# Performance work log

Measured on AMD Instinct MI355X. Metric: run time of the kernel, lower is better.

The kernel has to match this reference:

```python
import jax, jax.numpy as jnp
import numpy as np

N, E, F, C, K, H = 100000, 1600000, 64, 32, 8, 36


def setup_inputs() -> dict:
    key = jax.random.key(0)
    ks = jax.random.split(key, 24)
    s = 0.1
    inp = {
        "x": jax.random.normal(ks[0], (N, F), jnp.float32),
        "edge_index": jax.random.randint(ks[1], (2, E), 0, N, dtype=jnp.int32),
        # ChebConv conv1_1: K x [F, H] weights + bias
        "W1_1": jax.random.normal(ks[2], (K, F, H), jnp.float32) * s,
        "b1_1": jnp.zeros((H,), jnp.float32),
        "g1_1": jnp.ones((H,), jnp.float32),
        "be1_1": jnp.zeros((H,), jnp.float32),
        # ChebConv conv1_2: K x [H, H]
        "W1_2": jax.random.normal(ks[3], (K, H, H), jnp.float32) * s,
        "b1_2": jnp.zeros((H,), jnp.float32),
        "g1_2": jnp.ones((H,), jnp.float32),
        "be1_2": jnp.zeros((H,), jnp.float32),
        # GINConv MLP: Linear(F,H) -> ReLU -> Linear(H,H)
        "gin_w1": jax.random.normal(ks[4], (F, H), jnp.float32) * s,
        "gin_b1": jnp.zeros((H,), jnp.float32),
        "gin_w2": jax.random.normal(ks[5], (H, H), jnp.float32) * s,
        "gin_b2": jnp.zeros((H,), jnp.float32),
        "g2": jnp.ones((H,), jnp.float32),
        "be2": jnp.zeros((H,), jnp.float32),
        # conv4: ChebConv K=1 on concat(3H) -> C  (pure linear, no propagation)
        "W4": jax.random.normal(ks[6], (1, 3 * H, C), jnp.float32) * s,
        "b4": jnp.zeros((C,), jnp.float32),
    }
    return inp


def _spmm(w, src, dst, x, n):
    # out[i] = sum_{e: dst_e=i} w_e * x[src_e]
    return jax.ops.segment_sum(w[:, None] * x[src], dst, num_segments=n)


def _cheb(x, src, dst, w, Wk, b):
    # PyG ChebConv with sym norm, lambda_max=2: L_hat = -D^-1/2 A D^-1/2 (loop weight 0)
    n = x.shape[0]
    Kk = Wk.shape[0]
    Tx0 = x
    out = Tx0 @ Wk[0]
    if Kk > 1:
        Tx1 = _spmm(w, src, dst, Tx0, n)
        out = out + Tx1 @ Wk[1]
        for k in range(2, Kk):
            Tx2 = 2.0 * _spmm(w, src, dst, Tx1, n) - Tx0
            out = out + Tx2 @ Wk[k]
            Tx0, Tx1 = Tx1, Tx2
    return out + b


def _bn(x, g, b, eps=1e-5):
    m = jnp.mean(x, axis=0)
    v = jnp.mean(jnp.square(x - m), axis=0)  # biased var, training-mode BN
    return g * (x - m) * jax.lax.rsqrt(v + eps) + b


def reference(x, edge_index, W1_1, b1_1, g1_1, be1_1, W1_2, b1_2, g1_2, be1_2,
              gin_w1, gin_b1, gin_w2, gin_b2, g2, be2, W4, b4):
    src, dst = edge_index[0], edge_index[1]
    n = x.shape[0]
    deg = jax.ops.segment_sum(jnp.ones((src.shape[0],), x.dtype), src, num_segments=n)
    dis = jnp.where(deg > 0, jax.lax.rsqrt(jnp.maximum(deg, 1.0)), 0.0)
    w = -dis[src] * dis[dst]  # scaled Laplacian edge weights

    x1_1 = jax.nn.relu(_bn(_cheb(x, src, dst, w, W1_1, b1_1), g1_1, be1_1))
    x1_2 = jax.nn.relu(_bn(_cheb(x1_1, src, dst, w, W1_2, b1_2), g1_2, be1_2))

    # GINConv (eps=0): nn(x + sum_{j in N(i)} x_j)
    agg = jax.ops.segment_sum(x[src], dst, num_segments=n)
    h = x + agg
    gin = jax.nn.relu(h @ gin_w1 + gin_b1) @ gin_w2 + gin_b2
    x2 = _bn(jax.nn.relu(gin), g2, be2)

    x4 = jnp.concatenate((x1_1, x1_2, x2), axis=1)
    return x4 @ W4[0] + b4
```

## Files before the change

### kernel.cpp

```cpp
#include <hip/hip_runtime.h>

constexpr int N_NODES = 100000;
constexpr int N_EDGES = 1600000;
constexpr int NBK  = 391;
constexpr int NBLK = 640;
constexpr int CHUNK = 2500;
constexpr int LCNT = NBK * NBLK;
constexpr int SCAN_BLKS = (LCNT + 255) / 256;


__device__ __forceinline__ unsigned bf16pack(float a, float b) {
    unsigned ua = __float_as_uint(a), ub = __float_as_uint(b);
    ua += 0x7fffu + ((ua >> 16) & 1u);
    ub += 0x7fffu + ((ub >> 16) & 1u);
    return (ua >> 16) | (ub & 0xffff0000u);
}
__device__ __forceinline__ float bflo(unsigned p) { return __uint_as_float(p << 16); }
__device__ __forceinline__ float bfhi(unsigned p) { return __uint_as_float(p & 0xffff0000u); }

__device__ __forceinline__ int esrc(unsigned v) { return (int)(v & 0x1FFFFu); }
__device__ __forceinline__ float ew(unsigned v) {
    return __uint_as_float(0x80000000u | ((v >> 17) << 16));
}

__device__ __forceinline__ size_t sidx(int c, int row) {
    return (c < 8) ? ((size_t)row * 8 + c) : ((size_t)N_NODES * 8 + row);
}


__global__ __launch_bounds__(256) void part_count_kernel(
    const int* __restrict__ ei, int* __restrict__ cntD, int* __restrict__ cntS) {
    __shared__ int hd[NBK], hs[NBK];
    int tid = threadIdx.x;
    for (int i = tid; i < NBK; i += 256) { hd[i] = 0; hs[i] = 0; }
    __syncthreads();
    int e0 = blockIdx.x * CHUNK;
    for (int e = e0 + tid; e < e0 + CHUNK; e += 256) {
        int s = ei[e], d = ei[N_EDGES + e];
        atomicAdd(&hs[s >> 8], 1);
        atomicAdd(&hd[d >> 8], 1);
    }
    __syncthreads();
    for (int i = tid; i < NBK; i += 256) {
        cntD[i * NBLK + blockIdx.x] = hd[i];
        cntS[i * NBLK + blockIdx.x] = hs[i];
    }
}

__global__ __launch_bounds__(256) void scanA_kernel(const int* __restrict__ in,
                                                    int* __restrict__ out,
                                                    int* __restrict__ bsum, int L) {
    __shared__ int sm[256];
    int i = blockIdx.x * 256 + threadIdx.x;
    int v = (i < L) ? in[i] : 0;
    sm[threadIdx.x] = v;
    __syncthreads();
    for (int off = 1; off < 256; off <<= 1) {
        int t = (threadIdx.x >= off) ? sm[threadIdx.x - off] : 0;
        __syncthreads();
        sm[threadIdx.x] += t;
        __syncthreads();
    }
    if (i < L) out[i] = sm[threadIdx.x] - v;
    if (threadIdx.x == 255) bsum[blockIdx.x] = sm[255];
}

__global__ __launch_bounds__(1024) void scanB_kernel(int* __restrict__ bsum, int nb) {
    __shared__ int sm[1024];
    int t = threadIdx.x;
    int v = (t < nb) ? bsum[t] : 0;
    sm[t] = v;
    __syncthreads();
    for (int off = 1; off < 1024; off <<= 1) {
        int u = (t >= off) ? sm[t - off] : 0;
        __syncthreads();
        sm[t] += u;
        __syncthreads();
    }
    if (t < nb) bsum[t] = sm[t] - v;
}

__global__ __launch_bounds__(256) void scanC_kernel(int* __restrict__ out,
                                                    const int* __restrict__ bsum, int L) {
    int i = blockIdx.x * 256 + threadIdx.x;
    if (i < L) out[i] += bsum[blockIdx.x];
}

__global__ __launch_bounds__(256) void part_scatter_kernel(
    const int* __restrict__ ei, const int* __restrict__ scanD,
    const int* __restrict__ scanS, int2* __restrict__ edgepart,
    int* __restrict__ srcpart) {
    __shared__ int curD[NBK], curS[NBK];
    int tid = threadIdx.x;
    for (int i = tid; i < NBK; i += 256) {
        curD[i] = scanD[i * NBLK + blockIdx.x];
        curS[i] = scanS[i * NBLK + blockIdx.x];
    }
    __syncthreads();
    int e0 = blockIdx.x * CHUNK;
    for (int e = e0 + tid; e < e0 + CHUNK; e += 256) {
        int s = ei[e], d = ei[N_EDGES + e];
        int pd = atomicAdd(&curD[d >> 8], 1);
        edgepart[pd] = make_int2(s, d);
        int ps = atomicAdd(&curS[s >> 8], 1);
        srcpart[ps] = s;
    }
}

__global__ __launch_bounds__(256) void deg_kernel(const int* __restrict__ srcpart,
                                                  const int* __restrict__ scanS,
                                                  float* __restrict__ dis) {
    __shared__ int cnt[256];
    int b = blockIdx.x, tid = threadIdx.x;
    cnt[tid] = 0;
    __syncthreads();
    int beg = scanS[b * NBLK];
    int end = (b + 1 < NBK) ? scanS[(b + 1) * NBLK] : N_EDGES;
    for (int j = beg + tid; j < end; j += 256)
        atomicAdd(&cnt[srcpart[j] & 255], 1);
    __syncthreads();
    int node = b * 256 + tid;
    if (node < N_NODES) dis[node] = cnt[tid] > 0 ? rsqrtf((float)cnt[tid]) : 0.f;
}

__global__ __launch_bounds__(256) void csr_kernel(const int2* __restrict__ edgepart,
                                                  const int* __restrict__ scanD,
                                                  const float* __restrict__ dis,
                                                  int* __restrict__ rp,
                                                  unsigned* __restrict__ csrc) {
    __shared__ int cnt[256];
    __shared__ int lofs[256];
    __shared__ float disl[256];
    int b = blockIdx.x, tid = threadIdx.x;
    int beg = scanD[b * NBLK];
    int end = (b + 1 < NBK) ? scanD[(b + 1) * NBLK] : N_EDGES;
    int node = b * 256 + tid;
    cnt[tid] = 0;
    disl[tid] = (node < N_NODES) ? dis[node] : 0.f;
    __syncthreads();
    for (int j = beg + tid; j < end; j += 256)
        atomicAdd(&cnt[edgepart[j].y & 255], 1);
    __syncthreads();
    int v = cnt[tid];
    lofs[tid] = v;
    __syncthreads();
    for (int off = 1; off < 256; off <<= 1) {
        int t = (tid >= off) ? lofs[tid - off] : 0;
        __syncthreads();
        lofs[tid] += t;
        __syncthreads();
    }
    int myexc = lofs[tid] - v;
    if (node < N_NODES) rp[node] = beg + myexc;
    if (b == NBK - 1 && tid == 0) rp[N_NODES] = N_EDGES;
    __syncthreads();
    lofs[tid] = myexc;
    cnt[tid] = 0;
    __syncthreads();
    for (int j = beg + tid; j < end; j += 256) {
        int2 e = edgepart[j];
        int dl = e.y & 255;
        int pos = beg + lofs[dl] + atomicAdd(&cnt[dl], 1);
        unsigned u = __float_as_uint(-(dis[e.x] * disl[dl]));
        u += 0x7fffu + ((u >> 16) & 1u);
        unsigned wb = (u >> 16) & 0x7FFFu;
        csrc[pos] = (unsigned)e.x | (wb << 17);
    }
}

__global__ void pack_x_kernel(const float* __restrict__ x, uint2* __restrict__ xbf) {
    int i = blockIdx.x * blockDim.x + threadIdx.x;
    if (i >= N_NODES * 16) return;
    float4 v = ((const float4*)x)[i];
    xbf[i] = make_uint2(bf16pack(v.x, v.y), bf16pack(v.z, v.w));
}


template <int FI, int SCALE, bool HAS_B2, bool BN_A, bool FUSE_STATS>
__global__ __launch_bounds__(256) void cheb_step_kernel(
    const int* __restrict__ rp, const unsigned* __restrict__ csrc,
    const unsigned long long* __restrict__ INb, const unsigned long long* __restrict__ B2b,
    const unsigned long long* __restrict__ Ab, const float* __restrict__ W,
    const float* __restrict__ ss, unsigned long long* __restrict__ OUT,
    float* __restrict__ partials) {
    constexpr int RU2 = FI / 4;
    __shared__ float Wl[FI * 36];
    __shared__ float Atile[28][FI + 1];
    __shared__ float ls[72];
    int tid = threadIdx.x;
    for (int i = tid; i < FI * 36; i += 252) Wl[i] = W[i];
    int r0 = blockIdx.x * 28;
    for (int i = tid; i < 28 * RU2; i += 252) {
        int r = i / RU2, u = i % RU2;
        int row = r0 + r;
        long long av = 0;
        if (row < N_NODES) {
            size_t idx = (FI == 64) ? ((size_t)row * 16 + u) : sidx(u, row);
            av = (long long)Ab[idx];
        }
        unsigned lo = (unsigned)av, hi = (unsigned)(av >> 32);
        float f0 = bflo(lo), f1 = bfhi(lo), f2 = bflo(hi), f3 = bfhi(hi);
        if (BN_A) {
            int f = u * 4;
            f0 = fmaxf(fmaf(ss[f + 0], f0, ss[36 + f + 0]), 0.f);
            f1 = fmaxf(fmaf(ss[f + 1], f1, ss[36 + f + 1]), 0.f);
            f2 = fmaxf(fmaf(ss[f + 2], f2, ss[36 + f + 2]), 0.f);
            f3 = fmaxf(fmaf(ss[f + 3], f3, ss[36 + f + 3]), 0.f);
        }
        Atile[r][u * 4 + 0] = f0; Atile[r][u * 4 + 1] = f1;
        Atile[r][u * 4 + 2] = f2; Atile[r][u * 4 + 3] = f3;
    }
    if (FUSE_STATS && tid < 72) ls[tid] = 0.f;
    __syncthreads();
    int r = tid / 9, c = tid % 9;
    int row = r0 + r;
    bool valid = row < N_NODES;
    const unsigned long long* gb = INb + ((c < 8) ? (size_t)c : (size_t)N_NODES * 8);
    int gsh = (c < 8) ? 3 : 0;
    float ax = 0, ay = 0, az = 0, aw = 0;
    float bx = 0, by = 0, bz = 0, bw = 0;
    float cx = 0, cy = 0, cz = 0, cw = 0;
    float dx = 0, dy = 0, dz = 0, dw = 0;
    if (SCALE != 0 && valid) {
        int beg = rp[row], end = rp[row + 1];
        int j = beg;
        for (; j + 7 < end; j += 8) {
            unsigned v0 = csrc[j],     v1 = csrc[j + 1], v2 = csrc[j + 2], v3 = csrc[j + 3];
            unsigned v4 = csrc[j + 4], v5 = csrc[j + 5], v6 = csrc[j + 6], v7 = csrc[j + 7];
            unsigned long long q0 = gb[(size_t)esrc(v0) << gsh];
            unsigned long long q1 = gb[(size_t)esrc(v1) << gsh];
            unsigned long long q2 = gb[(size_t)esrc(v2) << gsh];
            unsigned long long q3 = gb[(size_t)esrc(v3) << gsh];
            unsigned long long q4 = gb[(size_t)esrc(v4) << gsh];
            unsigned long long q5 = gb[(size_t)esrc(v5) << gsh];
            unsigned long long q6 = gb[(size_t)esrc(v6) << gsh];
            unsigned long long q7 = gb[(size_t)esrc(v7) << gsh];
            float w0 = ew(v0), w1 = ew(v1), w2 = ew(v2), w3 = ew(v3);
            float w4 = ew(v4), w5 = ew(v5), w6 = ew(v6), w7 = ew(v7);
            unsigned l0 = (unsigned)q0, h0 = (unsigned)(q0 >> 32);
            unsigned l1 = (unsigned)q1, h1 = (unsigned)(q1 >> 32);
            unsigned l2 = (unsigned)q2, h2 = (unsigned)(q2 >> 32);
            unsigned l3 = (unsigned)q3, h3 = (unsigned)(q3 >> 32);
            unsigned l4 = (unsigned)q4, h4 = (unsigned)(q4 >> 32);
            unsigned l5 = (unsigned)q5, h5 = (unsigned)(q5 >> 32);
            unsigned l6 = (unsigned)q6, h6 = (unsigned)(q6 >> 32);
            unsigned l7 = (unsigned)q7, h7 = (unsigned)(q7 >> 32);
            ax = fmaf(w0, bflo(l0), ax); ay = fmaf(w0, bfhi(l0), ay);
            az = fmaf(w0, bflo(h0), az); aw = fmaf(w0, bfhi(h0), aw);
            bx = fmaf(w1, bflo(l1), bx); by = fmaf(w1, bfhi(l1), by);
            bz = fmaf(w1, bflo(h1), bz); bw = fmaf(w1, bfhi(h1), bw);
            cx = fmaf(w2, bflo(l2), cx); cy = fmaf(w2, bfhi(l2), cy);
            cz = fmaf(w2, bflo(h2), cz); cw = fmaf(w2, bfhi(h2), cw);
            dx = fmaf(w3, bflo(l3), dx); dy = fmaf(w3, bfhi(l3), dy);
            dz = fmaf(w3, bflo(h3), dz); dw = fmaf(w3, bfhi(h3), dw);
            ax = fmaf(w4, bflo(l4), ax); ay = fmaf(w4, bfhi(l4), ay);
            az = fmaf(w4, bflo(h4), az); aw = fmaf(w4, bfhi(h4), aw);
            bx = fmaf(w5, bflo(l5), bx); by = fmaf(w5, bfhi(l5), by);
            bz = fmaf(w5, bflo(h5), bz); bw = fmaf(w5, bfhi(h5), bw);
            cx = fmaf(w6, bflo(l6), cx); cy = fmaf(w6, bfhi(l6), cy);
            cz = fmaf(w6, bflo(h6), cz); cw = fmaf(w6, bfhi(h6), cw);
            dx = fmaf(w7, bflo(l7), dx); dy = fmaf(w7, bfhi(l7), dy);
            dz = fmaf(w7, bflo(h7), dz); dw = fmaf(w7, bfhi(h7), dw);
        }
        for (; j < end; ++j) {
            unsigned v = csrc[j];
            unsigned long long q = gb[(size_t)esrc(v) << gsh];
            float w = ew(v);
            unsigned l = (unsigned)q, h = (unsigned)(q >> 32);
            ax = fmaf(w, bflo(l), ax); ay = fmaf(w, bfhi(l), ay);
            az = fmaf(w, bflo(h), az); aw = fmaf(w, bfhi(h), aw);
        }
        ax += bx + cx + dx; ay += by + cy + dy;
        az += bz + cz + dz; aw += bw + cw + dw;
    }
    float px = 0, py = 0, pz = 0, pw = 0;
    const float4* Wl4 = (const float4*)Wl;
#pragma unroll 4
    for (int f = 0; f < FI; ++f) {
        float a = Atile[r][f];
        float4 wv = Wl4[f * 9 + c];
        px = fmaf(a, wv.x, px); py = fmaf(a, wv.y, py);
        pz = fmaf(a, wv.z, pz); pw = fmaf(a, wv.w, pw);
    }
    const float S = (float)SCALE;
    float4 o;
    o.x = fmaf(S, ax, px); o.y = fmaf(S, ay, py);
    o.z = fmaf(S, az, pz); o.w = fmaf(S, aw, pw);
    if (valid) {
        if (HAS_B2) {
            unsigned long long q = B2b[sidx(c, row)];
            unsigned l = (unsigned)q, h = (unsigned)(q >> 32);
            o.x -= bflo(l); o.y -= bfhi(l);
            o.z -= bflo(h); o.w -= bfhi(h);
        }
        unsigned long long pv = (unsigned long long)bf16pack(o.x, o.y)
                              | ((unsigned long long)bf16pack(o.z, o.w) << 32);
        OUT[sidx(c, row)] = pv;
        if (FUSE_STATS) {
            atomicAdd(&ls[c * 4 + 0], o.x); atomicAdd(&ls[36 + c * 4 + 0], o.x * o.x);
            atomicAdd(&ls[c * 4 + 1], o.y); atomicAdd(&ls[36 + c * 4 + 1], o.y * o.y);
            atomicAdd(&ls[c * 4 + 2], o.z); atomicAdd(&ls[36 + c * 4 + 2], o.z * o.z);
            atomicAdd(&ls[c * 4 + 3], o.w); atomicAdd(&ls[36 + c * 4 + 3], o.w * o.w);
        }
    }
    if (FUSE_STATS) {
        __syncthreads();
        if (tid < 72) partials[blockIdx.x * 72 + tid] = ls[tid];
    }
}


__global__ __launch_bounds__(256) void gin_gather_kernel(
    const int* __restrict__ rp, const unsigned* __restrict__ csrc,
    const unsigned long long* __restrict__ Yb, const float* __restrict__ b1,
    const float* __restrict__ w2, const float* __restrict__ b2,
    unsigned long long* __restrict__ OUT, float* __restrict__ partials) {
    __shared__ float W2l[36 * 36];
    __shared__ float B1l[36], B2l[36];
    __shared__ float M1t[28][37];
    __shared__ float ls[72];
    int tid = threadIdx.x;
    for (int i = tid; i < 36 * 36; i += 252) W2l[i] = w2[i];
    if (tid < 36) { B1l[tid] = b1[tid]; B2l[tid] = b2[tid]; }
    if (tid < 72) ls[tid] = 0.f;
    __syncthreads();
    int r = tid / 9, c = tid % 9;
    int row = blockIdx.x * 28 + r;
    bool valid = row < N_NODES;
    const unsigned long long* gb = Yb + ((c < 8) ? (size_t)c : (size_t)N_NODES * 8);
    int gsh = (c < 8) ? 3 : 0;
    float ax = 0, ay = 0, az = 0, aw = 0;
    float bx = 0, by = 0, bz = 0, bw = 0;
    float cx = 0, cy = 0, cz = 0, cw = 0;
    float dx = 0, dy = 0, dz = 0, dw = 0;
    if (valid) {
        unsigned long long qs = Yb[sidx(c, row)];
        unsigned lsf = (unsigned)qs, hsf = (unsigned)(qs >> 32);
        ax = bflo(lsf); ay = bfhi(lsf); az = bflo(hsf); aw = bfhi(hsf);
        int beg = rp[row], end = rp[row + 1];
        int j = beg;
        for (; j + 7 < end; j += 8) {
            unsigned long long q0 = gb[(size_t)esrc(csrc[j])     << gsh];
            unsigned long long q1 = gb[(size_t)esrc(csrc[j + 1]) << gsh];
            unsigned long long q2 = gb[(size_t)esrc(csrc[j + 2]) << gsh];
            unsigned long long q3 = gb[(size_t)esrc(csrc[j + 3]) << gsh];
            unsigned long long q4 = gb[(size_t)esrc(csrc[j + 4]) << gsh];
            unsigned long long q5 = gb[(size_t)esrc(csrc[j + 5]) << gsh];
            unsigned long long q6 = gb[(size_t)esrc(csrc[j + 6]) << gsh];
            unsigned long long q7 = gb[(size_t)esrc(csrc[j + 7]) << gsh];
            unsigned l0 = (unsigned)q0, h0 = (unsigned)(q0 >> 32);
            unsigned l1 = (unsigned)q1, h1 = (unsigned)(q1 >> 32);
            unsigned l2 = (unsigned)q2, h2 = (unsigned)(q2 >> 32);
            unsigned l3 = (unsigned)q3, h3 = (unsigned)(q3 >> 32);
            unsigned l4 = (unsigned)q4, h4 = (unsigned)(q4 >> 32);
            unsigned l5 = (unsigned)q5, h5 = (unsigned)(q5 >> 32);
            unsigned l6 = (unsigned)q6, h6 = (unsigned)(q6 >> 32);
            unsigned l7 = (unsigned)q7, h7 = (unsigned)(q7 >> 32);
            ax += bflo(l0) + bflo(l4); ay += bfhi(l0) + bfhi(l4);
            az += bflo(h0) + bflo(h4); aw += bfhi(h0) + bfhi(h4);
            bx += bflo(l1) + bflo(l5); by += bfhi(l1) + bfhi(l5);
            bz += bflo(h1) + bflo(h5); bw += bfhi(h1) + bfhi(h5);
            cx += bflo(l2) + bflo(l6); cy += bfhi(l2) + bfhi(l6);
            cz += bflo(h2) + bflo(h6); cw += bfhi(h2) + bfhi(h6);
            dx += bflo(l3) + bflo(l7); dy += bfhi(l3) + bfhi(l7);
            dz += bflo(h3) + bflo(h7); dw += bfhi(h3) + bfhi(h7);
        }
        for (; j < end; ++j) {
            unsigned long long q = gb[(size_t)esrc(csrc[j]) << gsh];
            unsigned l = (unsigned)q, h = (unsigned)(q >> 32);
            ax += bflo(l); ay += bfhi(l);
            az += bflo(h); aw += bfhi(h);
        }
        ax += bx + cx + dx; ay += by + cy + dy;
        az += bz + cz + dz; aw += bw + cw + dw;
    }
    float m0 = fmaxf(ax + B1l[c * 4 + 0], 0.f);
    float m1 = fmaxf(ay + B1l[c * 4 + 1], 0.f);
    float m2 = fmaxf(az + B1l[c * 4 + 2], 0.f);
    float m3 = fmaxf(aw + B1l[c * 4 + 3], 0.f);
    M1t[r][c * 4 + 0] = m0; M1t[r][c * 4 + 1] = m1;
    M1t[r][c * 4 + 2] = m2; M1t[r][c * 4 + 3] = m3;
    __syncthreads();
    float o0 = B2l[c * 4 + 0], o1 = B2l[c * 4 + 1];
    float o2 = B2l[c * 4 + 2], o3 = B2l[c * 4 + 3];
    const float4* W2l4 = (const float4*)W2l;
#pragma unroll 4
    for (int f = 0; f < 36; ++f) {
        float a = M1t[r][f];
        float4 wv = W2l4[f * 9 + c];
        o0 = fmaf(a, wv.x, o0); o1 = fmaf(a, wv.y, o1);
        o2 = fmaf(a, wv.z, o2); o3 = fmaf(a, wv.w, o3);
    }
    o0 = fmaxf(o0, 0.f); o1 = fmaxf(o1, 0.f);
    o2 = fmaxf(o2, 0.f); o3 = fmaxf(o3, 0.f);
    if (valid) {
        unsigned long long pv = (unsigned long long)bf16pack(o0, o1)
                              | ((unsigned long long)bf16pack(o2, o3) << 32);
        OUT[sidx(c, row)] = pv;
        atomicAdd(&ls[c * 4 + 0], o0); atomicAdd(&ls[36 + c * 4 + 0], o0 * o0);
        atomicAdd(&ls[c * 4 + 1], o1); atomicAdd(&ls[36 + c * 4 + 1], o1 * o1);
        atomicAdd(&ls[c * 4 + 2], o2); atomicAdd(&ls[36 + c * 4 + 2], o2 * o2);
        atomicAdd(&ls[c * 4 + 3], o3); atomicAdd(&ls[36 + c * 4 + 3], o3 * o3);
    }
    __syncthreads();
    if (tid < 72) partials[blockIdx.x * 72 + tid] = ls[tid];
}


__global__ __launch_bounds__(256) void finalize_kernel(
    const float* __restrict__ partials, int nb, const float* __restrict__ g,
    const float* __restrict__ be, float* __restrict__ ss) {
    __shared__ float rs[256], rq[256];
    int c = blockIdx.x;
    int t = threadIdx.x;
    float s = 0.f, q = 0.f;
    for (int i = t; i < nb; i += 256) {
        s += partials[i * 72 + c];
        q += partials[i * 72 + c + 36];
    }
    rs[t] = s; rq[t] = q;
    __syncthreads();
    for (int off = 128; off > 0; off >>= 1) {
        if (t < off) { rs[t] += rs[t + off]; rq[t] += rq[t + off]; }
        __syncthreads();
    }
    if (t == 0) {
        float m = rs[0] / (float)N_NODES;
        float v = rq[0] / (float)N_NODES - m * m;
        float sc = g[c] * rsqrtf(v + 1e-5f);
        ss[c] = sc;
        ss[36 + c] = be[c] - m * sc;
    }
}


__global__ __launch_bounds__(256) void fused3_kernel(
    const unsigned long long* __restrict__ X1b, const float* __restrict__ ssA,
    const unsigned long long* __restrict__ X2b, const float* __restrict__ ssB,
    const unsigned long long* __restrict__ X3b, const float* __restrict__ ssC,
    const float* __restrict__ W, const float* __restrict__ b,
    float* __restrict__ out) {
    __shared__ float Wl[108 * 32];
    __shared__ float Al[32][109];
    int tid = threadIdx.x;
    for (int i = tid; i < 108 * 32; i += 256) Wl[i] = W[i];
    int r0 = blockIdx.x * 32;
    for (int i = tid; i < 32 * 108; i += 256) {
        int r = i / 108, f = i % 108;
        int row = r0 + r;
        float v = 0.f;
        if (row < N_NODES) {
            int t = f / 36, ff = f % 36;
            const unsigned short* b16 =
                (const unsigned short*)(t == 0 ? X1b : (t == 1 ? X2b : X3b));
            unsigned short u16 = (ff < 32)
                ? b16[(size_t)row * 32 + ff]
                : b16[(size_t)N_NODES * 32 + (size_t)row * 4 + (ff - 32)];
            float xv = __uint_as_float((unsigned)u16 << 16);
            if (t == 0)      v = fmaxf(fmaf(ssA[ff], xv, ssA[36 + ff]), 0.f);
            else if (t == 1) v = fmaxf(fmaf(ssB[ff], xv, ssB[36 + ff]), 0.f);
            else             v = fmaf(ssC[ff], xv, ssC[36 + ff]);
        }
        Al[r][f] = v;
    }
    __syncthreads();
    int r = tid >> 3, q = tid & 7;
    int row = r0 + r;
    if (row >= N_NODES) return;
    float acc[4];
#pragma unroll
    for (int j = 0; j < 4; ++j) acc[j] = b[q * 4 + j];
    for (int f = 0; f < 108; ++f) {
        float a = Al[r][f];
#pragma unroll
        for (int j = 0; j < 4; ++j)
            acc[j] = fmaf(a, Wl[f * 32 + q * 4 + j], acc[j]);
    }
#pragma unroll
    for (int j = 0; j < 4; ++j) out[(size_t)row * 32 + q * 4 + j] = acc[j];
}


extern "C" void kernel_launch(void* const* d_in, const int* in_sizes, int n_in,
                              void* d_out, int out_size, void* d_ws, size_t ws_size,
                              hipStream_t stream) {
    const float* x      = (const float*)d_in[0];
    const int*   ei     = (const int*)d_in[1];
    const float* W1_1   = (const float*)d_in[2];
    const float* g1_1   = (const float*)d_in[4];
    const float* be1_1  = (const float*)d_in[5];
    const float* W1_2   = (const float*)d_in[6];
    const float* g1_2   = (const float*)d_in[8];
    const float* be1_2  = (const float*)d_in[9];
    const float* gin_w1 = (const float*)d_in[10];
    const float* gin_b1 = (const float*)d_in[11];
    const float* gin_w2 = (const float*)d_in[12];
    const float* gin_b2 = (const float*)d_in[13];
    const float* g2     = (const float*)d_in[14];
    const float* be2    = (const float*)d_in[15];
    const float* W4     = (const float*)d_in[16];
    const float* b4     = (const float*)d_in[17];
    float* out = (float*)d_out;

    char* ws = (char*)d_ws;
    size_t off = 0;
    auto alloc = [&](size_t bytes) -> char* {
        char* p = ws + off;
        off = (off + bytes + 255) & ~(size_t)255;
        return p;
    };
    int*   cntD  = (int*)alloc((size_t)LCNT * 4);
    int*   cntS  = (int*)alloc((size_t)LCNT * 4);
    int*   bsum  = (int*)alloc(1024 * 4);
    int*   rp    = (int*)alloc((size_t)(N_NODES + 1) * 4);
    float* dis   = (float*)alloc((size_t)N_NODES * 4);
    int2*  edgepart = (int2*)alloc((size_t)N_EDGES * 8);
    int*   srcpart  = (int*)alloc((size_t)N_EDGES * 4);
    unsigned* csrc = (unsigned*)alloc((size_t)N_EDGES * 4);
    float* ssA   = (float*)alloc(72 * 4);
    float* ssB   = (float*)alloc(72 * 4);
    float* ssC   = (float*)alloc(72 * 4);
    float* partials = (float*)alloc((size_t)6250 * 72 * 4);
    constexpr size_t NBBF = (size_t)N_NODES * 72;
    uint2* xbf = (uint2*)alloc((size_t)N_NODES * 128);
    unsigned long long* R0  = (unsigned long long*)alloc(NBBF);
    unsigned long long* R1  = (unsigned long long*)alloc(NBBF);
    unsigned long long* R2  = (unsigned long long*)alloc(NBBF);
    unsigned long long* X1b = (unsigned long long*)alloc(NBBF);
    unsigned long long* X2b = (unsigned long long*)alloc(NBBF);
    unsigned long long* X3b = (unsigned long long*)alloc(NBBF);
    if (off > ws_size) return;

    part_count_kernel<<<NBLK, 256, 0, stream>>>(ei, cntD, cntS);
    scanA_kernel<<<SCAN_BLKS, 256, 0, stream>>>(cntD, cntD, bsum, LCNT);
    scanB_kernel<<<1, 1024, 0, stream>>>(bsum, SCAN_BLKS);
    scanC_kernel<<<SCAN_BLKS, 256, 0, stream>>>(cntD, bsum, LCNT);
    scanA_kernel<<<SCAN_BLKS, 256, 0, stream>>>(cntS, cntS, bsum, LCNT);
    scanB_kernel<<<1, 1024, 0, stream>>>(bsum, SCAN_BLKS);
    scanC_kernel<<<SCAN_BLKS, 256, 0, stream>>>(cntS, bsum, LCNT);
    part_scatter_kernel<<<NBLK, 256, 0, stream>>>(ei, cntD, cntS, edgepart, srcpart);
    deg_kernel<<<NBK, 256, 0, stream>>>(srcpart, cntS, dis);
    csr_kernel<<<NBK, 256, 0, stream>>>(edgepart, cntD, dis, rp, csrc);
    pack_x_kernel<<<(N_NODES * 16 + 255) / 256, 256, 0, stream>>>(x, xbf);

    const int STEP_BLKS = (N_NODES + 27) / 28;
    const int F3_BLKS   = (N_NODES + 31) / 32;
    const unsigned long long* xb64 = (const unsigned long long*)xbf;

    cheb_step_kernel<64, 0, false, false, false><<<STEP_BLKS, 252, 0, stream>>>(
        rp, csrc, nullptr, nullptr, xb64, W1_1 + 7 * 2304, nullptr, R0, nullptr);
    cheb_step_kernel<64, 2, false, false, false><<<STEP_BLKS, 252, 0, stream>>>(
        rp, csrc, R0, nullptr, xb64, W1_1 + 6 * 2304, nullptr, R1, nullptr);
    cheb_step_kernel<64, 2, true, false, false><<<STEP_BLKS, 252, 0, stream>>>(
        rp, csrc, R1, R0, xb64, W1_1 + 5 * 2304, nullptr, R2, nullptr);
    cheb_step_kernel<64, 2, true, false, false><<<STEP_BLKS, 252, 0, stream>>>(
        rp, csrc, R2, R1, xb64, W1_1 + 4 * 2304, nullptr, R0, nullptr);
    cheb_step_kernel<64, 2, true, false, false><<<STEP_BLKS, 252, 0, stream>>>(
        rp, csrc, R0, R2, xb64, W1_1 + 3 * 2304, nullptr, R1, nullptr);
    cheb_step_kernel<64, 2, true, false, false><<<STEP_BLKS, 252, 0, stream>>>(
        rp, csrc, R1, R0, xb64, W1_1 + 2 * 2304, nullptr, R2, nullptr);
    cheb_step_kernel<64, 2, true, false, false><<<STEP_BLKS, 252, 0, stream>>>(
        rp, csrc, R2, R1, xb64, W1_1 + 1 * 2304, nullptr, R0, nullptr);
    cheb_step_kernel<64, 1, true, false, true><<<STEP_BLKS, 252, 0, stream>>>(
        rp, csrc, R0, R2, xb64, W1_1 + 0 * 2304, nullptr, X1b, partials);
    finalize_kernel<<<36, 256, 0, stream>>>(partials, STEP_BLKS, g1_1, be1_1, ssA);

    cheb_step_kernel<36, 0, false, true, false><<<STEP_BLKS, 252, 0, stream>>>(
        rp, csrc, nullptr, nullptr, X1b, W1_2 + 7 * 1296, ssA, R0, nullptr);
    cheb_step_kernel<36, 2, false, true, false><<<STEP_BLKS, 252, 0, stream>>>(
        rp, csrc, R0, nullptr, X1b, W1_2 + 6 * 1296, ssA, R1, nullptr);
    cheb_step_kernel<36, 2, true, true, false><<<STEP_BLKS, 252, 0, stream>>>(
        rp, csrc, R1, R0, X1b, W1_2 + 5 * 1296, ssA, R2, nullptr);
    cheb_step_kernel<36, 2, true, true, false><<<STEP_BLKS, 252, 0, stream>>>(
        rp, csrc, R2, R1, X1b, W1_2 + 4 * 1296, ssA, R0, nullptr);
    cheb_step_kernel<36, 2, true, true, false><<<STEP_BLKS, 252, 0, stream>>>(
        rp, csrc, R0, R2, X1b, W1_2 + 3 * 1296, ssA, R1, nullptr);
    cheb_step_kernel<36, 2, true, true, false><<<STEP_BLKS, 252, 0, stream>>>(
        rp, csrc, R1, R0, X1b, W1_2 + 2 * 1296, ssA, R2, nullptr);
    cheb_step_kernel<36, 2, true, true, false><<<STEP_BLKS, 252, 0, stream>>>(
        rp, csrc, R2, R1, X1b, W1_2 + 1 * 1296, ssA, R0, nullptr);
    cheb_step_kernel<36, 1, true, true, true><<<STEP_BLKS, 252, 0, stream>>>(
        rp, csrc, R0, R2, X1b, W1_2 + 0 * 1296, ssA, X2b, partials);
    finalize_kernel<<<36, 256, 0, stream>>>(partials, STEP_BLKS, g1_2, be1_2, ssB);

    cheb_step_kernel<64, 0, false, false, false><<<STEP_BLKS, 252, 0, stream>>>(
        rp, csrc, nullptr, nullptr, xb64, gin_w1, nullptr, R0, nullptr);
    gin_gather_kernel<<<STEP_BLKS, 252, 0, stream>>>(rp, csrc, R0, gin_b1,
                                                     gin_w2, gin_b2, X3b, partials);
    finalize_kernel<<<36, 256, 0, stream>>>(partials, STEP_BLKS, g2, be2, ssC);

    fused3_kernel<<<F3_BLKS, 256, 0, stream>>>(X1b, ssA, X2b, ssB, X3b, ssC, W4, b4, out);
}
```

Measured before the change: 906.8 us.

## Batch all Chebyshev projections into one kernel and make Clenshaw steps pure gathers

Each layer's per-step dense projection (A·W_k) now runs once up front in a batched projection kernel that writes all K projected tensors, including the GIN first linear, to a workspace. The Clenshaw recurrence steps become lightweight gather kernels that add the precomputed projection instead of reloading the A tile and weights every step. The GIN path is reordered to project first, then aggregate, then apply the second linear. The prepass scratch buffers are aliased into the new projection workspace. This cuts repeated GEMM and weight-load work per step, in exchange for extra memory traffic to write and reread the projection tensors.

Result: slower. 926.0 us (+2.1%).

```diff
diff --git a/kernel.cpp b/kernel.cpp
--- a/kernel.cpp
+++ b/kernel.cpp
@@ -7,6 +7,7 @@
 constexpr int CHUNK = 2500;
 constexpr int LCNT = NBK * NBLK;
 constexpr int SCAN_BLKS = (LCNT + 255) / 256;
+constexpr size_t YST = (size_t)N_NODES * 9;
 
 
 __device__ __forceinline__ unsigned bf16pack(float a, float b) {
@@ -176,19 +177,18 @@
 }
 
 
-template <int FI, int SCALE, bool HAS_B2, bool BN_A, bool FUSE_STATS>
-__global__ __launch_bounds__(256) void cheb_step_kernel(
-    const int* __restrict__ rp, const unsigned* __restrict__ csrc,
-    const unsigned long long* __restrict__ INb, const unsigned long long* __restrict__ B2b,
+template <int FI, int NK, bool BN_A, bool EXTRA, bool BIAS_RELU, bool FUSE_STATS>
+__global__ __launch_bounds__(256) void batchproj_kernel(
     const unsigned long long* __restrict__ Ab, const float* __restrict__ W,
-    const float* __restrict__ ss, unsigned long long* __restrict__ OUT,
+    const float* __restrict__ Wx, const float* __restrict__ ss,
+    const float* __restrict__ bias, unsigned long long* __restrict__ Y,
     float* __restrict__ partials) {
     constexpr int RU2 = FI / 4;
+    constexpr int NKT = NK + (EXTRA ? 1 : 0);
     __shared__ float Wl[FI * 36];
     __shared__ float Atile[28][FI + 1];
     __shared__ float ls[72];
     int tid = threadIdx.x;
-    for (int i = tid; i < FI * 36; i += 252) Wl[i] = W[i];
     int r0 = blockIdx.x * 28;
     for (int i = tid; i < 28 * RU2; i += 252) {
         int r = i / RU2, u = i % RU2;
@@ -211,17 +211,68 @@
         Atile[r][u * 4 + 2] = f2; Atile[r][u * 4 + 3] = f3;
     }
     if (FUSE_STATS && tid < 72) ls[tid] = 0.f;
-    __syncthreads();
     int r = tid / 9, c = tid % 9;
     int row = r0 + r;
-    bool valid = row < N_NODES;
+    for (int kk = 0; kk < NKT; ++kk) {
+        const float* Wk = (EXTRA && kk == NK) ? Wx : (W + (size_t)kk * FI * 36);
+        __syncthreads();
+        for (int i = tid; i < FI * 36; i += 252) Wl[i] = Wk[i];
+        __syncthreads();
+        float px = 0, py = 0, pz = 0, pw = 0;
+        const float4* Wl4 = (const float4*)Wl;
+#pragma unroll 4
+        for (int f = 0; f < FI; ++f) {
+            float a = Atile[r][f];
+            float4 wv = Wl4[f * 9 + c];
+            px = fmaf(a, wv.x, px); py = fmaf(a, wv.y, py);
+            pz = fmaf(a, wv.z, pz); pw = fmaf(a, wv.w, pw);
+        }
+        if (BIAS_RELU) {
+            int cb = c * 4;
+            px = fmaxf(px + bias[cb + 0], 0.f); py = fmaxf(py + bias[cb + 1], 0.f);
+            pz = fmaxf(pz + bias[cb + 2], 0.f); pw = fmaxf(pw + bias[cb + 3], 0.f);
+        }
+        if (row < N_NODES) {
+            unsigned long long pv = (unsigned long long)bf16pack(px, py)
+                                  | ((unsigned long long)bf16pack(pz, pw) << 32);
+            Y[(size_t)kk * YST + sidx(c, row)] = pv;
+            if (FUSE_STATS) {
+                atomicAdd(&ls[c * 4 + 0], px); atomicAdd(&ls[36 + c * 4 + 0], px * px);
+                atomicAdd(&ls[c * 4 + 1], py); atomicAdd(&ls[36 + c * 4 + 1], py * py);
+                atomicAdd(&ls[c * 4 + 2], pz); atomicAdd(&ls[36 + c * 4 + 2], pz * pz);
+                atomicAdd(&ls[c * 4 + 3], pw); atomicAdd(&ls[36 + c * 4 + 3], pw * pw);
+            }
+        }
+    }
+    if (FUSE_STATS) {
+        __syncthreads();
+        if (tid < 72) partials[(size_t)blockIdx.x * 72 + tid] = ls[tid];
+    }
+}
+
+
+template <int SCALE, bool WEIGHTED, bool HAS_B2, bool BIAS_RELU, bool FUSE_STATS>
+__global__ __launch_bounds__(256) void gstep_kernel(
+    const int* __restrict__ rp, const unsigned* __restrict__ csrc,
+    const unsigned long long* __restrict__ INb, const unsigned long long* __restrict__ Yk,
+    const unsigned long long* __restrict__ B2b, const float* __restrict__ bias,
+    unsigned long long* __restrict__ OUT, float* __restrict__ partials) {
+    __shared__ float ls[72];
+    int tid = threadIdx.x;
+    if (FUSE_STATS) { if (tid < 72) ls[tid] = 0.f; __syncthreads(); }
+    int r = tid / 9, c = tid % 9;
+    int row = blockIdx.x * 28 + r;
+    if (row >= N_NODES) {
+        if (FUSE_STATS) { __syncthreads(); if (tid < 72) partials[(size_t)blockIdx.x * 72 + tid] = ls[tid]; }
+        return;
+    }
     const unsigned long long* gb = INb + ((c < 8) ? (size_t)c : (size_t)N_NODES * 8);
     int gsh = (c < 8) ? 3 : 0;
     float ax = 0, ay = 0, az = 0, aw = 0;
     float bx = 0, by = 0, bz = 0, bw = 0;
     float cx = 0, cy = 0, cz = 0, cw = 0;
     float dx = 0, dy = 0, dz = 0, dw = 0;
-    if (SCALE != 0 && valid) {
+    {
         int beg = rp[row], end = rp[row + 1];
         int j = beg;
         for (; j + 7 < end; j += 8) {
@@ -235,8 +286,6 @@
             unsigned long long q5 = gb[(size_t)esrc(v5) << gsh];
             unsigned long long q6 = gb[(size_t)esrc(v6) << gsh];
             unsigned long long q7 = gb[(size_t)esrc(v7) << gsh];
-            float w0 = ew(v0), w1 = ew(v1), w2 = ew(v2), w3 = ew(v3);
-            float w4 = ew(v4), w5 = ew(v5), w6 = ew(v6), w7 = ew(v7);
             unsigned l0 = (unsigned)q0, h0 = (unsigned)(q0 >> 32);
             unsigned l1 = (unsigned)q1, h1 = (unsigned)(q1 >> 32);
             unsigned l2 = (unsigned)q2, h2 = (unsigned)(q2 >> 32);
@@ -245,165 +294,79 @@
             unsigned l5 = (unsigned)q5, h5 = (unsigned)(q5 >> 32);
             unsigned l6 = (unsigned)q6, h6 = (unsigned)(q6 >> 32);
             unsigned l7 = (unsigned)q7, h7 = (unsigned)(q7 >> 32);
-            ax = fmaf(w0, bflo(l0), ax); ay = fmaf(w0, bfhi(l0), ay);
-            az = fmaf(w0, bflo(h0), az); aw = fmaf(w0, bfhi(h0), aw);
-            bx = fmaf(w1, bflo(l1), bx); by = fmaf(w1, bfhi(l1), by);
-            bz = fmaf(w1, bflo(h1), bz); bw = fmaf(w1, bfhi(h1), bw);
-            cx = fmaf(w2, bflo(l2), cx); cy = fmaf(w2, bfhi(l2), cy);
-            cz = fmaf(w2, bflo(h2), cz); cw = fmaf(w2, bfhi(h2), cw);
-            dx = fmaf(w3, bflo(l3), dx); dy = fmaf(w3, bfhi(l3), dy);
-            dz = fmaf(w3, bflo(h3), dz); dw = fmaf(w3, bfhi(h3), dw);
-            ax = fmaf(w4, bflo(l4), ax); ay = fmaf(w4, bfhi(l4), ay);
-            az = fmaf(w4, bflo(h4), az); aw = fmaf(w4, bfhi(h4), aw);
-            bx = fmaf(w5, bflo(l5), bx); by = fmaf(w5, bfhi(l5), by);
-            bz = fmaf(w5, bflo(h5), bz); bw = fmaf(w5, bfhi(h5), bw);
-            cx = fmaf(w6, bflo(l6), cx); cy = fmaf(w6, bfhi(l6), cy);
-            cz = fmaf(w6, bflo(h6), cz); cw = fmaf(w6, bfhi(h6), cw);
-            dx = fmaf(w7, bflo(l7), dx); dy = fmaf(w7, bfhi(l7), dy);
-            dz = fmaf(w7, bflo(h7), dz); dw = fmaf(w7, bfhi(h7), dw);
+            if (WEIGHTED) {
+                float w0 = ew(v0), w1 = ew(v1), w2 = ew(v2), w3 = ew(v3);
+                float w4 = ew(v4), w5 = ew(v5), w6 = ew(v6), w7 = ew(v7);
+                ax = fmaf(w0, bflo(l0), ax); ay = fmaf(w0, bfhi(l0), ay);
+                az = fmaf(w0, bflo(h0), az); aw = fmaf(w0, bfhi(h0), aw);
+                bx = fmaf(w1, bflo(l1), bx); by = fmaf(w1, bfhi(l1), by);
+                bz = fmaf(w1, bflo(h1), bz); bw = fmaf(w1, bfhi(h1), bw);
+                cx = fmaf(w2, bflo(l2), cx); cy = fmaf(w2, bfhi(l2), cy);
+                cz = fmaf(w2, bflo(h2), cz); cw = fmaf(w2, bfhi(h2), cw);
+                dx = fmaf(w3, bflo(l3), dx); dy = fmaf(w3, bfhi(l3), dy);
+                dz = fmaf(w3, bflo(h3), dz); dw = fmaf(w3, bfhi(h3), dw);
+                ax = fmaf(w4, bflo(l4), ax); ay = fmaf(w4, bfhi(l4), ay);
+                az = fmaf(w4, bflo(h4), az); aw = fmaf(w4, bfhi(h4), aw);
+                bx = fmaf(w5, bflo(l5), bx); by = fmaf(w5, bfhi(l5), by);
+                bz = fmaf(w5, bflo(h5), bz); bw = fmaf(w5, bfhi(h5), bw);
+                cx = fmaf(w6, bflo(l6), cx); cy = fmaf(w6, bfhi(l6), cy);
+                cz = fmaf(w6, bflo(h6), cz); cw = fmaf(w6, bfhi(h6), cw);
+                dx = fmaf(w7, bflo(l7), dx); dy = fmaf(w7, bfhi(l7), dy);
+                dz = fmaf(w7, bflo(h7), dz); dw = fmaf(w7, bfhi(h7), dw);
+            } else {
+                ax += bflo(l0) + bflo(l4); ay += bfhi(l0) + bfhi(l4);
+                az += bflo(h0) + bflo(h4); aw += bfhi(h0) + bfhi(h4);
+                bx += bflo(l1) + bflo(l5); by += bfhi(l1) + bfhi(l5);
+                bz += bflo(h1) + bflo(h5); bw += bfhi(h1) + bfhi(h5);
+                cx += bflo(l2) + bflo(l6); cy += bfhi(l2) + bfhi(l6);
+                cz += bflo(h2) + bflo(h6); cw += bfhi(h2) + bfhi(h6);
+                dx += bflo(l3) + bflo(l7); dy += bfhi(l3) + bfhi(l7);
+                dz += bflo(h3) + bflo(h7); dw += bfhi(h3) + bfhi(h7);
+            }
         }
         for (; j < end; ++j) {
             unsigned v = csrc[j];
             unsigned long long q = gb[(size_t)esrc(v) << gsh];
-            float w = ew(v);
             unsigned l = (unsigned)q, h = (unsigned)(q >> 32);
-            ax = fmaf(w, bflo(l), ax); ay = fmaf(w, bfhi(l), ay);
-            az = fmaf(w, bflo(h), az); aw = fmaf(w, bfhi(h), aw);
+            if (WEIGHTED) {
+                float w = ew(v);
+                ax = fmaf(w, bflo(l), ax); ay = fmaf(w, bfhi(l), ay);
+                az = fmaf(w, bflo(h), az); aw = fmaf(w, bfhi(h), aw);
+            } else {
+                ax += bflo(l); ay += bfhi(l);
+                az += bflo(h); aw += bfhi(h);
+            }
         }
         ax += bx + cx + dx; ay += by + cy + dy;
         az += bz + cz + dz; aw += bw + cw + dw;
     }
-    float px = 0, py = 0, pz = 0, pw = 0;
-    const float4* Wl4 = (const float4*)Wl;
-#pragma unroll 4
-    for (int f = 0; f < FI; ++f) {
-        float a = Atile[r][f];
-        float4 wv = Wl4[f * 9 + c];
-        px = fmaf(a, wv.x, px); py = fmaf(a, wv.y, py);
-        pz = fmaf(a, wv.z, pz); pw = fmaf(a, wv.w, pw);
-    }
     const float S = (float)SCALE;
-    float4 o;
-    o.x = fmaf(S, ax, px); o.y = fmaf(S, ay, py);
-    o.z = fmaf(S, az, pz); o.w = fmaf(S, aw, pw);
-    if (valid) {
-        if (HAS_B2) {
-            unsigned long long q = B2b[sidx(c, row)];
-            unsigned l = (unsigned)q, h = (unsigned)(q >> 32);
-            o.x -= bflo(l); o.y -= bfhi(l);
-            o.z -= bflo(h); o.w -= bfhi(h);
-        }
-        unsigned long long pv = (unsigned long long)bf16pack(o.x, o.y)
-                              | ((unsigned long long)bf16pack(o.z, o.w) << 32);
-        OUT[sidx(c, row)] = pv;
-        if (FUSE_STATS) {
-            atomicAdd(&ls[c * 4 + 0], o.x); atomicAdd(&ls[36 + c * 4 + 0], o.x * o.x);
-            atomicAdd(&ls[c * 4 + 1], o.y); atomicAdd(&ls[36 + c * 4 + 1], o.y * o.y);
-            atomicAdd(&ls[c * 4 + 2], o.z); atomicAdd(&ls[36 + c * 4 + 2], o.z * o.z);
-            atomicAdd(&ls[c * 4 + 3], o.w); atomicAdd(&ls[36 + c * 4 + 3], o.w * o.w);
-        }
-    }
+    unsigned long long qy = Yk[sidx(c, row)];
+    unsigned ly = (unsigned)qy, hy = (unsigned)(qy >> 32);
+    float ox = fmaf(S, ax, bflo(ly)), oy = fmaf(S, ay, bfhi(ly));
+    float oz = fmaf(S, az, bflo(hy)), ow = fmaf(S, aw, bfhi(hy));
+    if (HAS_B2) {
+        unsigned long long qb = B2b[sidx(c, row)];
+        unsigned lb = (unsigned)qb, hb = (unsigned)(qb >> 32);
+        ox -= bflo(lb); oy -= bfhi(lb);
+        oz -= bflo(hb); ow -= bfhi(hb);
+    }
+    if (BIAS_RELU) {
+        int cb = c * 4;
+        ox = fmaxf(ox + bias[cb + 0], 0.f); oy = fmaxf(oy + bias[cb + 1], 0.f);
+        oz = fmaxf(oz + bias[cb + 2], 0.f); ow = fmaxf(ow + bias[cb + 3], 0.f);
+    }
+    unsigned long long pv = (unsigned long long)bf16pack(ox, oy)
+                          | ((unsigned long long)bf16pack(oz, ow) << 32);
+    OUT[sidx(c, row)] = pv;
     if (FUSE_STATS) {
-        __syncthreads();
-        if (tid < 72) partials[blockIdx.x * 72 + tid] = ls[tid];
-    }
-}
-
-
-__global__ __launch_bounds__(256) void gin_gather_kernel(
-    const int* __restrict__ rp, const unsigned* __restrict__ csrc,
-    const unsigned long long* __restrict__ Yb, const float* __restrict__ b1,
-    const float* __restrict__ w2, const float* __restrict__ b2,
-    unsigned long long* __restrict__ OUT, float* __restrict__ partials) {
-    __shared__ float W2l[36 * 36];
-    __shared__ float B1l[36], B2l[36];
-    __shared__ float M1t[28][37];
-    __shared__ float ls[72];
-    int tid = threadIdx.x;
-    for (int i = tid; i < 36 * 36; i += 252) W2l[i] = w2[i];
-    if (tid < 36) { B1l[tid] = b1[tid]; B2l[tid] = b2[tid]; }
-    if (tid < 72) ls[tid] = 0.f;
-    __syncthreads();
-    int r = tid / 9, c = tid % 9;
-    int row = blockIdx.x * 28 + r;
-    bool valid = row < N_NODES;
-    const unsigned long long* gb = Yb + ((c < 8) ? (size_t)c : (size_t)N_NODES * 8);
-    int gsh = (c < 8) ? 3 : 0;
-    float ax = 0, ay = 0, az = 0, aw = 0;
-    float bx = 0, by = 0, bz = 0, bw = 0;
-    float cx = 0, cy = 0, cz = 0, cw = 0;
-    float dx = 0, dy = 0, dz = 0, dw = 0;
-    if (valid) {
-        unsigned long long qs = Yb[sidx(c, row)];
-        unsigned lsf = (unsigned)qs, hsf = (unsigned)(qs >> 32);
-        ax = bflo(lsf); ay = bfhi(lsf); az = bflo(hsf); aw = bfhi(hsf);
-        int beg = rp[row], end = rp[row + 1];
-        int j = beg;
-        for (; j + 7 < end; j += 8) {
-            unsigned long long q0 = gb[(size_t)esrc(csrc[j])     << gsh];
-            unsigned long long q1 = gb[(size_t)esrc(csrc[j + 1]) << gsh];
-            unsigned long long q2 = gb[(size_t)esrc(csrc[j + 2]) << gsh];
-            unsigned long long q3 = gb[(size_t)esrc(csrc[j + 3]) << gsh];
-            unsigned long long q4 = gb[(size_t)esrc(csrc[j + 4]) << gsh];
-            unsigned long long q5 = gb[(size_t)esrc(csrc[j + 5]) << gsh];
-            unsigned long long q6 = gb[(size_t)esrc(csrc[j + 6]) << gsh];
-            unsigned long long q7 = gb[(size_t)esrc(csrc[j + 7]) << gsh];
-            unsigned l0 = (unsigned)q0, h0 = (unsigned)(q0 >> 32);
-            unsigned l1 = (unsigned)q1, h1 = (unsigned)(q1 >> 32);
-            unsigned l2 = (unsigned)q2, h2 = (unsigned)(q2 >> 32);
-            unsigned l3 = (unsigned)q3, h3 = (unsigned)(q3 >> 32);
-            unsigned l4 = (unsigned)q4, h4 = (unsigned)(q4 >> 32);
-            unsigned l5 = (unsigned)q5, h5 = (unsigned)(q5 >> 32);
-            unsigned l6 = (unsigned)q6, h6 = (unsigned)(q6 >> 32);
-            unsigned l7 = (unsigned)q7, h7 = (unsigned)(q7 >> 32);
-            ax += bflo(l0) + bflo(l4); ay += bfhi(l0) + bfhi(l4);
-            az += bflo(h0) + bflo(h4); aw += bfhi(h0) + bfhi(h4);
-            bx += bflo(l1) + bflo(l5); by += bfhi(l1) + bfhi(l5);
-            bz += bflo(h1) + bflo(h5); bw += bfhi(h1) + bfhi(h5);
-            cx += bflo(l2) + bflo(l6); cy += bfhi(l2) + bfhi(l6);
-            cz += bflo(h2) + bflo(h6); cw += bfhi(h2) + bfhi(h6);
-            dx += bflo(l3) + bflo(l7); dy += bfhi(l3) + bfhi(l7);
-            dz += bflo(h3) + bflo(h7); dw += bfhi(h3) + bfhi(h7);
-        }
-        for (; j < end; ++j) {
-            unsigned long long q = gb[(size_t)esrc(csrc[j]) << gsh];
-            unsigned l = (unsigned)q, h = (unsigned)(q >> 32);
-            ax += bflo(l); ay += bfhi(l);
-            az += bflo(h); aw += bfhi(h);
-        }
-        ax += bx + cx + dx; ay += by + cy + dy;
-        az += bz + cz + dz; aw += bw + cw + dw;
-    }
-    float m0 = fmaxf(ax + B1l[c * 4 + 0], 0.f);
-    float m1 = fmaxf(ay + B1l[c * 4 + 1], 0.f);
-    float m2 = fmaxf(az + B1l[c * 4 + 2], 0.f);
-    float m3 = fmaxf(aw + B1l[c * 4 + 3], 0.f);
-    M1t[r][c * 4 + 0] = m0; M1t[r][c * 4 + 1] = m1;
-    M1t[r][c * 4 + 2] = m2; M1t[r][c * 4 + 3] = m3;
-    __syncthreads();
-    float o0 = B2l[c * 4 + 0], o1 = B2l[c * 4 + 1];
-    float o2 = B2l[c * 4 + 2], o3 = B2l[c * 4 + 3];
-    const float4* W2l4 = (const float4*)W2l;
-#pragma unroll 4
-    for (int f = 0; f < 36; ++f) {
-        float a = M1t[r][f];
-        float4 wv = W2l4[f * 9 + c];
-        o0 = fmaf(a, wv.x, o0); o1 = fmaf(a, wv.y, o1);
-        o2 = fmaf(a, wv.z, o2); o3 = fmaf(a, wv.w, o3);
-    }
-    o0 = fmaxf(o0, 0.f); o1 = fmaxf(o1, 0.f);
-    o2 = fmaxf(o2, 0.f); o3 = fmaxf(o3, 0.f);
-    if (valid) {
-        unsigned long long pv = (unsigned long long)bf16pack(o0, o1)
-                              | ((unsigned long long)bf16pack(o2, o3) << 32);
-        OUT[sidx(c, row)] = pv;
-        atomicAdd(&ls[c * 4 + 0], o0); atomicAdd(&ls[36 + c * 4 + 0], o0 * o0);
-        atomicAdd(&ls[c * 4 + 1], o1); atomicAdd(&ls[36 + c * 4 + 1], o1 * o1);
-        atomicAdd(&ls[c * 4 + 2], o2); atomicAdd(&ls[36 + c * 4 + 2], o2 * o2);
-        atomicAdd(&ls[c * 4 + 3], o3); atomicAdd(&ls[36 + c * 4 + 3], o3 * o3);
-    }
-    __syncthreads();
-    if (tid < 72) partials[blockIdx.x * 72 + tid] = ls[tid];
+        atomicAdd(&ls[c * 4 + 0], ox); atomicAdd(&ls[36 + c * 4 + 0], ox * ox);
+        atomicAdd(&ls[c * 4 + 1], oy); atomicAdd(&ls[36 + c * 4 + 1], oy * oy);
+        atomicAdd(&ls[c * 4 + 2], oz); atomicAdd(&ls[36 + c * 4 + 2], oz * oz);
+        atomicAdd(&ls[c * 4 + 3], ow); atomicAdd(&ls[36 + c * 4 + 3], ow * ow);
+        __syncthreads();
+        if (tid < 72) partials[(size_t)blockIdx.x * 72 + tid] = ls[tid];
+    }
 }
 
 
@@ -415,8 +378,8 @@
     int t = threadIdx.x;
     float s = 0.f, q = 0.f;
     for (int i = t; i < nb; i += 256) {
-        s += partials[i * 72 + c];
-        q += partials[i * 72 + c + 36];
+        s += partials[(size_t)i * 72 + c];
+        q += partials[(size_t)i * 72 + c + 36];
     }
     rs[t] = s; rq[t] = q;
     __syncthreads();
@@ -509,20 +472,16 @@
         off = (off + bytes + 255) & ~(size_t)255;
         return p;
     };
-    int*   cntD  = (int*)alloc((size_t)LCNT * 4);
-    int*   cntS  = (int*)alloc((size_t)LCNT * 4);
-    int*   bsum  = (int*)alloc(1024 * 4);
     int*   rp    = (int*)alloc((size_t)(N_NODES + 1) * 4);
-    float* dis   = (float*)alloc((size_t)N_NODES * 4);
-    int2*  edgepart = (int2*)alloc((size_t)N_EDGES * 8);
-    int*   srcpart  = (int*)alloc((size_t)N_EDGES * 4);
     unsigned* csrc = (unsigned*)alloc((size_t)N_EDGES * 4);
     float* ssA   = (float*)alloc(72 * 4);
     float* ssB   = (float*)alloc(72 * 4);
     float* ssC   = (float*)alloc(72 * 4);
     float* partials = (float*)alloc((size_t)6250 * 72 * 4);
+    uint2* xbf = (uint2*)alloc((size_t)N_NODES * 128);
+    char*  U = alloc(9 * YST * 8);
+    unsigned long long* Yall = (unsigned long long*)U;
     constexpr size_t NBBF = (size_t)N_NODES * 72;
-    uint2* xbf = (uint2*)alloc((size_t)N_NODES * 128);
     unsigned long long* R0  = (unsigned long long*)alloc(NBBF);
     unsigned long long* R1  = (unsigned long long*)alloc(NBBF);
     unsigned long long* R2  = (unsigned long long*)alloc(NBBF);
@@ -530,6 +489,13 @@
     unsigned long long* X2b = (unsigned long long*)alloc(NBBF);
     unsigned long long* X3b = (unsigned long long*)alloc(NBBF);
     if (off > ws_size) return;
+
+    int*   cntD = (int*)U;
+    int*   cntS = cntD + LCNT;
+    int*   bsum = cntS + LCNT;
+    float* dis  = (float*)(bsum + 1024);
+    int2*  edgepart = (int2*)(dis + N_NODES);
+    int*   srcpart  = (int*)(edgepart + N_EDGES);
 
     part_count_kernel<<<NBLK, 256, 0, stream>>>(ei, cntD, cntS);
     scanA_kernel<<<SCAN_BLKS, 256, 0, stream>>>(cntD, cntD, bsum, LCNT);
@@ -543,51 +509,52 @@
     csr_kernel<<<NBK, 256, 0, stream>>>(edgepart, cntD, dis, rp, csrc);
     pack_x_kernel<<<(N_NODES * 16 + 255) / 256, 256, 0, stream>>>(x, xbf);
 
-    const int STEP_BLKS = (N_NODES + 27) / 28;
-    const int F3_BLKS   = (N_NODES + 31) / 32;
+    const int BLKS = (N_NODES + 27) / 28;
+    const int F3_BLKS = (N_NODES + 31) / 32;
     const unsigned long long* xb64 = (const unsigned long long*)xbf;
-
-    cheb_step_kernel<64, 0, false, false, false><<<STEP_BLKS, 252, 0, stream>>>(
-        rp, csrc, nullptr, nullptr, xb64, W1_1 + 7 * 2304, nullptr, R0, nullptr);
-    cheb_step_kernel<64, 2, false, false, false><<<STEP_BLKS, 252, 0, stream>>>(
-        rp, csrc, R0, nullptr, xb64, W1_1 + 6 * 2304, nullptr, R1, nullptr);
-    cheb_step_kernel<64, 2, true, false, false><<<STEP_BLKS, 252, 0, stream>>>(
-        rp, csrc, R1, R0, xb64, W1_1 + 5 * 2304, nullptr, R2, nullptr);
-    cheb_step_kernel<64, 2, true, false, false><<<STEP_BLKS, 252, 0, stream>>>(
-        rp, csrc, R2, R1, xb64, W1_1 + 4 * 2304, nullptr, R0, nullptr);
-    cheb_step_kernel<64, 2, true, false, false><<<STEP_BLKS, 252, 0, stream>>>(
-        rp, csrc, R0, R2, xb64, W1_1 + 3 * 2304, nullptr, R1, nullptr);
-    cheb_step_kernel<64, 2, true, false, false><<<STEP_BLKS, 252, 0, stream>>>(
-        rp, csrc, R1, R0, xb64, W1_1 + 2 * 2304, nullptr, R2, nullptr);
-    cheb_step_kernel<64, 2, true, false, false><<<STEP_BLKS, 252, 0, stream>>>(
-        rp, csrc, R2, R1, xb64, W1_1 + 1 * 2304, nullptr, R0, nullptr);
-    cheb_step_kernel<64, 1, true, false, true><<<STEP_BLKS, 252, 0, stream>>>(
-        rp, csrc, R0, R2, xb64, W1_1 + 0 * 2304, nullptr, X1b, partials);
-    finalize_kernel<<<36, 256, 0, stream>>>(partials, STEP_BLKS, g1_1, be1_1, ssA);
-
-    cheb_step_kernel<36, 0, false, true, false><<<STEP_BLKS, 252, 0, stream>>>(
-        rp, csrc, nullptr, nullptr, X1b, W1_2 + 7 * 1296, ssA, R0, nullptr);
-    cheb_step_kernel<36, 2, false, true, false><<<STEP_BLKS, 252, 0, stream>>>(
-        rp, csrc, R0, nullptr, X1b, W1_2 + 6 * 1296, ssA, R1, nullptr);
-    cheb_step_kernel<36, 2, true, true, false><<<STEP_BLKS, 252, 0, stream>>>(
-        rp, csrc, R1, R0, X1b, W1_2 + 5 * 1296, ssA, R2, nullptr);
-    cheb_step_kernel<36, 2, true, true, false><<<STEP_BLKS, 252, 0, stream>>>(
-        rp, csrc, R2, R1, X1b, W1_2 + 4 * 1296, ssA, R0, nullptr);
-    cheb_step_kernel<36, 2, true, true, false><<<STEP_BLKS, 252, 0, stream>>>(
-        rp, csrc, R0, R2, X1b, W1_2 + 3 * 1296, ssA, R1, nullptr);
-    cheb_step_kernel<36, 2, true, true, false><<<STEP_BLKS, 252, 0, stream>>>(
-        rp, csrc, R1, R0, X1b, W1_2 + 2 * 1296, ssA, R2, nullptr);
-    cheb_step_kernel<36, 2, true, true, false><<<STEP_BLKS, 252, 0, stream>>>(
-        rp, csrc, R2, R1, X1b, W1_2 + 1 * 1296, ssA, R0, nullptr);
-    cheb_step_kernel<36, 1, true, true, true><<<STEP_BLKS, 252, 0, stream>>>(
-        rp, csrc, R0, R2, X1b, W1_2 + 0 * 1296, ssA, X2b, partials);
-    finalize_kernel<<<36, 256, 0, stream>>>(partials, STEP_BLKS, g1_2, be1_2, ssB);
-
-    cheb_step_kernel<64, 0, false, false, false><<<STEP_BLKS, 252, 0, stream>>>(
-        rp, csrc, nullptr, nullptr, xb64, gin_w1, nullptr, R0, nullptr);
-    gin_gather_kernel<<<STEP_BLKS, 252, 0, stream>>>(rp, csrc, R0, gin_b1,
-                                                     gin_w2, gin_b2, X3b, partials);
-    finalize_kernel<<<36, 256, 0, stream>>>(partials, STEP_BLKS, g2, be2, ssC);
+    auto Y = [&](int k) { return Yall + (size_t)k * YST; };
+
+    batchproj_kernel<64, 8, false, true, false, false><<<BLKS, 252, 0, stream>>>(
+        xb64, W1_1, gin_w1, nullptr, nullptr, Yall, nullptr);
+    gstep_kernel<2, true, false, false, false><<<BLKS, 252, 0, stream>>>(
+        rp, csrc, Y(7), Y(6), nullptr, nullptr, R0, nullptr);
+    gstep_kernel<2, true, true, false, false><<<BLKS, 252, 0, stream>>>(
+        rp, csrc, R0, Y(5), Y(7), nullptr, R1, nullptr);
+    gstep_kernel<2, true, true, false, false><<<BLKS, 252, 0, stream>>>(
+        rp, csrc, R1, Y(4), R0, nullptr, R2, nullptr);
+    gstep_kernel<2, true, true, false, false><<<BLKS, 252, 0, stream>>>(
+        rp, csrc, R2, Y(3), R1, nullptr, R0, nullptr);
+    gstep_kernel<2, true, true, false, false><<<BLKS, 252, 0, stream>>>(
+        rp, csrc, R0, Y(2), R2, nullptr, R1, nullptr);
+    gstep_kernel<2, true, true, false, false><<<BLKS, 252, 0, stream>>>(
+        rp, csrc, R1, Y(1), R0, nullptr, R2, nullptr);
+    gstep_kernel<1, true, true, false, true><<<BLKS, 252, 0, stream>>>(
+        rp, csrc, R2, Y(0), R1, nullptr, X1b, partials);
+    finalize_kernel<<<36, 256, 0, stream>>>(partials, BLKS, g1_1, be1_1, ssA);
+
+    gstep_kernel<1, false, false, true, false><<<BLKS, 252, 0, stream>>>(
+        rp, csrc, Y(8), Y(8), nullptr, gin_b1, R0, nullptr);
+    batchproj_kernel<36, 1, false, false, true, true><<<BLKS, 252, 0, stream>>>(
+        R0, gin_w2, nullptr, nullptr, gin_b2, X3b, partials);
+    finalize_kernel<<<36, 256, 0, stream>>>(partials, BLKS, g2, be2, ssC);
+
+    batchproj_kernel<36, 8, true, false, false, false><<<BLKS, 252, 0, stream>>>(
+        X1b, W1_2, nullptr, ssA, nullptr, Yall, nullptr);
+    gstep_kernel<2, true, false, false, false><<<BLKS, 252, 0, stream>>>(
+        rp, csrc, Y(7), Y(6), nullptr, nullptr, R0, nullptr);
+    gstep_kernel<2, true, true, false, false><<<BLKS, 252, 0, stream>>>(
+        rp, csrc, R0, Y(5), Y(7), nullptr, R1, nullptr);
+    gstep_kernel<2, true, true, false, false><<<BLKS, 252, 0, stream>>>(
+        rp, csrc, R1, Y(4), R0, nullptr, R2, nullptr);
+    gstep_kernel<2, true, true, false, false><<<BLKS, 252, 0, stream>>>(
+        rp, csrc, R2, Y(3), R1, nullptr, R0, nullptr);
+    gstep_kernel<2, true, true, false, false><<<BLKS, 252, 0, stream>>>(
+        rp, csrc, R0, Y(2), R2, nullptr, R1, nullptr);
+    gstep_kernel<2, true, true, false, false><<<BLKS, 252, 0, stream>>>(
+        rp, csrc, R1, Y(1), R0, nullptr, R2, nullptr);
+    gstep_kernel<1, true, true, false, true><<<BLKS, 252, 0, stream>>>(
+        rp, csrc, R2, Y(0), R1, nullptr, X2b, partials);
+    finalize_kernel<<<36, 256, 0, stream>>>(partials, BLKS, g1_2, be1_2, ssB);
 
     fused3_kernel<<<F3_BLKS, 256, 0, stream>>>(X1b, ssA, X2b, ssB, X3b, ssC, W4, b4, out);
 }
```
